# Optimization experiments

Hardware: AMD Instinct MI355X
Metric: run time of the kernel (lower is better)

## Reference

```python
import jax, jax.numpy as jnp
import numpy as np
from functools import partial

D_MODEL, D_INNER, D_STATE, DT_RANK, D_CONV, N_LAYER = 1024, 2048, 16, 64, 4, 4
OUT_DIM = 1024
EPS = 1e-5


def rmsnorm(x, w):
    return x * jax.lax.rsqrt(jnp.mean(x * x, axis=-1, keepdims=True) + EPS) * w


def causal_depthwise_conv(x, w, b):
    # x: [B, L, D]; w: [D, K]; depthwise causal conv along L
    xc = jnp.transpose(x, (0, 2, 1))  # [B, D, L]
    out = jax.lax.conv_general_dilated(
        xc, w[:, None, :],  # [D, 1, K]
        window_strides=(1,), padding=[(D_CONV - 1, 0)],
        dimension_numbers=('NCH', 'OIH', 'NCH'),
        feature_group_count=D_INNER)
    out = out + b[None, :, None]
    return jnp.transpose(out, (0, 2, 1))  # [B, L, D]


def selective_scan(u, delta, A, B, C, D):
    # u, delta: [b,l,d]; A: [d,n]; B,C: [b,l,n]; D: [d]
    def step(h, inp):
        d_t, B_t, C_t, u_t = inp  # [b,d],[b,n],[b,n],[b,d]
        dA = jnp.exp(d_t[..., None] * A)            # [b,d,n]
        h = dA * h + (d_t * u_t)[..., None] * B_t[:, None, :]
        y = jnp.einsum('bdn,bn->bd', h, C_t)
        return h, y
    b = u.shape[0]
    h0 = jnp.zeros((b, D_INNER, D_STATE), dtype=u.dtype)
    xs = (jnp.swapaxes(delta, 0, 1), jnp.swapaxes(B, 0, 1),
          jnp.swapaxes(C, 0, 1), jnp.swapaxes(u, 0, 1))
    _, ys = jax.lax.scan(step, h0, xs)
    y = jnp.swapaxes(ys, 0, 1)  # [b,l,d]
    return y + u * D


def mamba_block(x, in_w, conv_w, conv_b, xproj_w, dt_w, dt_b, A_log, D, out_w):
    xz = jnp.einsum('bld,ed->ble', x, in_w)            # [b,l,2*di]
    xp, z = jnp.split(xz, 2, axis=-1)
    xp = jax.nn.silu(causal_depthwise_conv(xp, conv_w, conv_b))
    x_dbl = jnp.einsum('bld,ed->ble', xp, xproj_w)      # [b,l,dt_rank+2n]
    dt, Bm, Cm = jnp.split(x_dbl, [DT_RANK, DT_RANK + D_STATE], axis=-1)
    delta = jax.nn.softplus(jnp.einsum('blr,dr->bld', dt, dt_w) + dt_b)
    A = -jnp.exp(A_log)
    y = selective_scan(xp, delta, A, Bm, Cm, D)
    y = y * jax.nn.silu(z)
    return jnp.einsum('bld,md->blm', y, out_w)


def setup_inputs() -> dict:
    key = jax.random.key(0)
    ks = jax.random.split(key, 16)
    s = 0.02
    x = jax.random.normal(ks[0], (2, 2048, D_MODEL), dtype=jnp.float32)
    emb_w = jax.random.normal(ks[1], (D_MODEL, D_MODEL), dtype=jnp.float32) * s
    emb_b = jnp.zeros((D_MODEL,), dtype=jnp.float32)
    L = N_LAYER
    in_proj_w = jax.random.normal(ks[2], (L, 2 * D_INNER, D_MODEL), dtype=jnp.float32) * s
    conv_w = jax.random.normal(ks[3], (L, D_INNER, D_CONV), dtype=jnp.float32) * 0.1
    conv_b = jnp.zeros((L, D_INNER), dtype=jnp.float32)
    x_proj_w = jax.random.normal(ks[4], (L, DT_RANK + 2 * D_STATE, D_INNER), dtype=jnp.float32) * s
    dt_proj_w = jax.random.normal(ks[5], (L, D_INNER, DT_RANK), dtype=jnp.float32) * s
    dt_proj_b = jax.random.uniform(ks[6], (L, D_INNER), dtype=jnp.float32, minval=-4.0, maxval=-2.0)
    A_log = jnp.broadcast_to(jnp.log(jnp.arange(1, D_STATE + 1, dtype=jnp.float32)), (L, D_INNER, D_STATE)).copy()
    D = jnp.ones((L, D_INNER), dtype=jnp.float32)
    out_proj_w = jax.random.normal(ks[7], (L, D_MODEL, D_INNER), dtype=jnp.float32) * s
    norm_w = jnp.ones((D_MODEL,), dtype=jnp.float32)
    head_w = jax.random.normal(ks[8], (OUT_DIM, D_MODEL), dtype=jnp.float32) * s
    return dict(x=x, emb_w=emb_w, emb_b=emb_b, in_proj_w=in_proj_w, conv_w=conv_w,
                conv_b=conv_b, x_proj_w=x_proj_w, dt_proj_w=dt_proj_w,
                dt_proj_b=dt_proj_b, A_log=A_log, D=D, out_proj_w=out_proj_w,
                norm_w=norm_w, head_w=head_w)


def reference(x, emb_w, emb_b, in_proj_w, conv_w, conv_b, x_proj_w, dt_proj_w,
              dt_proj_b, A_log, D, out_proj_w, norm_w, head_w):
    h = jnp.einsum('bli,di->bld', x, emb_w) + emb_b
    for i in range(N_LAYER):
        y = mamba_block(h, in_proj_w[i], conv_w[i], conv_b[i], x_proj_w[i],
                        dt_proj_w[i], dt_proj_b[i], A_log[i], D[i], out_proj_w[i])
        h = h + rmsnorm(y, norm_w)
    h = rmsnorm(h, norm_w)
    return jnp.einsum('bld,od->blo', h, head_w)
```

## Files before the change

### kernel.cpp

```cpp
#include <hip/hip_runtime.h>
#include <hip/hip_bf16.h>

#define DMODEL 1024
#define DINNER 2048
#define DSTATE 16
#define DTRANK 64
#define NLAYER 4
#define SEQ    2048
#define NB     2
#define BL     (NB*SEQ)

#define NCH   64
#define CLEN  (SEQ / NCH)

#define KSPLIT 8
#define NXD    96

typedef __bf16 bf16x8 __attribute__((ext_vector_type(8)));
typedef float  f32x4  __attribute__((ext_vector_type(4)));
typedef unsigned short u16x8 __attribute__((ext_vector_type(8)));

__device__ __forceinline__ unsigned short f2bf(float f) {
  unsigned int x = __builtin_bit_cast(unsigned int, f);
  x += 0x7fffu + ((x >> 16) & 1u);
  return (unsigned short)(x >> 16);
}
__device__ __forceinline__ float bf2f(unsigned short u) {
  unsigned int x = ((unsigned int)u) << 16;
  return __builtin_bit_cast(float, x);
}
__device__ __forceinline__ float siluf(float x) {
  return x * (1.f / (1.f + __expf(-x)));
}
__device__ __forceinline__ float softplusf(float x) {
  return (x > 15.f) ? x : __logf(1.f + __expf(x));
}

__device__ __forceinline__ void gload_lds16(const void* g, void* l) {
  __builtin_amdgcn_global_load_lds(
      (const __attribute__((address_space(1))) void*)g,
      (__attribute__((address_space(3))) void*)l, 16, 0, 0);
}

__device__ __forceinline__ void pack16(const float* p, u16x8& u0, u16x8& u1) {
  float4 f0 = *(const float4*)(p);
  float4 f1 = *(const float4*)(p + 4);
  float4 f2 = *(const float4*)(p + 8);
  float4 f3 = *(const float4*)(p + 12);
  u0[0]=f2bf(f0.x); u0[1]=f2bf(f0.y); u0[2]=f2bf(f0.z); u0[3]=f2bf(f0.w);
  u0[4]=f2bf(f1.x); u0[5]=f2bf(f1.y); u0[6]=f2bf(f1.z); u0[7]=f2bf(f1.w);
  u1[0]=f2bf(f2.x); u1[1]=f2bf(f2.y); u1[2]=f2bf(f2.z); u1[3]=f2bf(f2.w);
  u1[4]=f2bf(f3.x); u1[5]=f2bf(f3.y); u1[6]=f2bf(f3.z); u1[7]=f2bf(f3.w);
}

__global__ __launch_bounds__(512, 2) void gemm256(
    const unsigned short* __restrict__ A, int lda,
    const unsigned short* __restrict__ B, int ldb,
    unsigned short* __restrict__ Cbf, int ldc, int K)
{
  __shared__ alignas(16) unsigned short lds[3 * 16384];

  const int tid  = threadIdx.x;
  const int bm   = blockIdx.x, bn = blockIdx.y;
  const int wave = tid >> 6, lane = tid & 63;
  const int wm   = wave >> 2, wn = wave & 3;
  const int fr   = lane & 15, fq = lane >> 4;

  const int srow   = lane >> 2;
  const int schunk = (lane & 3) ^ ((lane >> 3) & 3);
  const unsigned short* Abase = A + (size_t)(bm * 256) * lda;
  const unsigned short* Bbase = B + (size_t)(bn * 256) * ldb;

  const int rc = fq ^ ((fr >> 1) & 3);

  f32x4 acc[8][4] = {};

#define STAGE256(t)                                                          \
  {                                                                          \
    char* sbase = (char*)lds + ((t) % 3) * 32768;                            \
    int k0 = (t) * 32;                                                       \
    _Pragma("unroll")                                                        \
    for (int r = 0; r < 2; ++r) {                                            \
      gload_lds16(Abase + (size_t)(r * 128 + wave * 16 + srow) * lda + k0 +  \
                      schunk * 8,                                            \
                  sbase + r * 8192 + wave * 1024);                           \
      gload_lds16(Bbase + (size_t)(r * 128 + wave * 16 + srow) * ldb + k0 +  \
                      schunk * 8,                                            \
                  sbase + 16384 + r * 8192 + wave * 1024);                   \
    }                                                                        \
  }

  const int NT = K >> 5;

  STAGE256(0);
  __builtin_amdgcn_sched_barrier(0);
  STAGE256(1);
  asm volatile("s_waitcnt vmcnt(4)" ::: "memory");
  __builtin_amdgcn_s_barrier();
  __builtin_amdgcn_sched_barrier(0);

  for (int t = 0; t < NT; ++t) {
    if (t + 2 < NT) STAGE256(t + 2);

    const char* bufp = (const char*)lds + (t % 3) * 32768;

    bf16x8 bfr[4];
#pragma unroll
    for (int nj = 0; nj < 4; ++nj)
      bfr[nj] = *(const bf16x8*)(bufp + 16384 +
                                 (wn * 64 + nj * 16 + fr) * 64 + rc * 16);
    __builtin_amdgcn_s_setprio(1);
#pragma unroll
    for (int mi = 0; mi < 8; ++mi) {
      bf16x8 af = *(const bf16x8*)(bufp + (wm * 128 + mi * 16 + fr) * 64 + rc * 16);
#pragma unroll
      for (int nj = 0; nj < 4; ++nj)
        acc[mi][nj] = __builtin_amdgcn_mfma_f32_16x16x32_bf16(af, bfr[nj], acc[mi][nj], 0, 0, 0);
    }
    __builtin_amdgcn_s_setprio(0);

    __builtin_amdgcn_sched_barrier(0);
    if (t + 2 < NT) {
      asm volatile("s_waitcnt vmcnt(4)" ::: "memory");
    } else if (t + 1 < NT) {
      asm volatile("s_waitcnt vmcnt(0)" ::: "memory");
    }
    __builtin_amdgcn_s_barrier();
    __builtin_amdgcn_sched_barrier(0);
  }
#undef STAGE256

#pragma unroll
  for (int mi = 0; mi < 8; ++mi)
#pragma unroll
    for (int nj = 0; nj < 4; ++nj)
#pragma unroll
      for (int q = 0; q < 4; ++q) {
        int row = bm * 256 + wm * 128 + mi * 16 + fq * 4 + q;
        int col = bn * 256 + wn * 64 + nj * 16 + fr;
        Cbf[(size_t)row * ldc + col] = f2bf(acc[mi][nj][q]);
      }
}

template<int ACT>
__global__ __launch_bounds__(256) void gemm_bf(
    const unsigned short* __restrict__ A, int lda,
    const unsigned short* __restrict__ B, int ldb,
    float* __restrict__ C, int ldc, int K,
    const float* __restrict__ bias,
    unsigned short* __restrict__ Cbf)
{
  __shared__ alignas(16) unsigned short ldsb[3 * 8192];

  const int tid  = threadIdx.x;
  const int bm   = blockIdx.x, bn = blockIdx.y;
  const int wave = tid >> 6,  lane = tid & 63;
  const int wm   = wave >> 1, wn   = wave & 1;
  const int fr   = lane & 15, fq   = lane >> 4;

  const int srow   = lane >> 2;
  const int schunk = (lane & 3) ^ ((lane >> 3) & 3);
  const unsigned short* Abase = A + (size_t)(bm * 128) * lda;
  const unsigned short* Bbase = B + (size_t)(bn * 128) * ldb;

  const int rc = fq ^ ((fr >> 1) & 3);

  f32x4 acc[4][4] = {};

#define STAGEP(t)                                                            \
  {                                                                          \
    char* sbase = (char*)ldsb + ((t) % 3) * 16384;                           \
    int k0 = (t) * 32;                                                       \
    _Pragma("unroll")                                                        \
    for (int j = 0; j < 2; ++j) {                                            \
      gload_lds16(Abase + (size_t)(wave * 32 + j * 16 + srow) * lda + k0 +   \
                      schunk * 8,                                            \
                  sbase + wave * 2048 + j * 1024);                           \
      gload_lds16(Bbase + (size_t)(wave * 32 + j * 16 + srow) * ldb + k0 +   \
                      schunk * 8,                                            \
                  sbase + 8192 + wave * 2048 + j * 1024);                    \
    }                                                                        \
  }

  const int NT = K >> 5;

  STAGEP(0);
  __builtin_amdgcn_sched_barrier(0);
  STAGEP(1);
  asm volatile("s_waitcnt vmcnt(4)" ::: "memory");
  __builtin_amdgcn_s_barrier();
  __builtin_amdgcn_sched_barrier(0);

  for (int t = 0; t < NT; ++t) {
    if (t + 2 < NT) STAGEP(t + 2);

    const char* bufp = (const char*)ldsb + (t % 3) * 16384;

    bf16x8 af[4], bfr[4];
#pragma unroll
    for (int mi = 0; mi < 4; ++mi)
      af[mi] = *(const bf16x8*)(bufp + (wm * 64 + mi * 16 + fr) * 64 + rc * 16);
#pragma unroll
    for (int nj = 0; nj < 4; ++nj)
      bfr[nj] = *(const bf16x8*)(bufp + 8192 +
                                 (wn * 64 + nj * 16 + fr) * 64 + rc * 16);
    __builtin_amdgcn_s_setprio(1);
#pragma unroll
    for (int mi = 0; mi < 4; ++mi)
#pragma unroll
      for (int nj = 0; nj < 4; ++nj)
        acc[mi][nj] = __builtin_amdgcn_mfma_f32_16x16x32_bf16(af[mi], bfr[nj], acc[mi][nj], 0, 0, 0);
    __builtin_amdgcn_s_setprio(0);

    __builtin_amdgcn_sched_barrier(0);
    if (t + 2 < NT) {
      asm volatile("s_waitcnt vmcnt(4)" ::: "memory");
    } else if (t + 1 < NT) {
      asm volatile("s_waitcnt vmcnt(0)" ::: "memory");
    }
    __builtin_amdgcn_s_barrier();
    __builtin_amdgcn_sched_barrier(0);
  }
#undef STAGEP

#pragma unroll
  for (int mi = 0; mi < 4; ++mi)
#pragma unroll
    for (int nj = 0; nj < 4; ++nj)
#pragma unroll
      for (int q = 0; q < 4; ++q) {
        int row = bm * 128 + wm * 64 + mi * 16 + fq * 4 + q;
        int col = bn * 128 + wn * 64 + nj * 16 + fr;
        float v = acc[mi][nj][q];
        if (bias) v += bias[col];
        if (ACT == 1) v = softplusf(v);
        if (C)   C[(size_t)row * ldc + col] = v;
        if (Cbf) Cbf[(size_t)row * ldc + col] = f2bf(v);
      }
}

__global__ __launch_bounds__(256) void gemm_xdbl(
    const unsigned short* __restrict__ A, const float* __restrict__ B,
    float* __restrict__ part)
{
  __shared__ alignas(16) unsigned short As[128 * 32];
  __shared__ alignas(16) unsigned short Bs[128 * 32];

  const int tid  = threadIdx.x;
  const int bm   = blockIdx.x;
  const int z    = blockIdx.z;
  const int wave = tid >> 6,  lane = tid & 63;
  const int wm   = wave >> 1, wn   = wave & 1;
  const int fr   = lane & 15, fq   = lane >> 4;

  const int r  = tid >> 1, hh = tid & 1;
  const int sw = (r & 7) << 4;
  const int offS0 = ((r * 64 + hh * 32)     ) ^ sw;
  const int offS1 = ((r * 64 + hh * 32 + 16)) ^ sw;

  const unsigned short* aRow = A + (size_t)(bm * 128 + r) * DINNER + hh * 16;
  const float* bRow = B + (size_t)r * DINNER + hh * 16;
  const bool bValid = (r < NXD);

  f32x4 acc[4][4] = {};

  const int kbeg = z * (DINNER / KSPLIT);
  for (int k0 = kbeg; k0 < kbeg + DINNER / KSPLIT; k0 += 32) {
    {
      u16x8 u0 = *(const u16x8*)(aRow + k0);
      u16x8 u1 = *(const u16x8*)(aRow + k0 + 8);
      *(u16x8*)((char*)As + offS0) = u0;
      *(u16x8*)((char*)As + offS1) = u1;
    }
    {
      u16x8 u0 = {}, u1 = {};
      if (bValid) pack16(bRow + k0, u0, u1);
      *(u16x8*)((char*)Bs + offS0) = u0;
      *(u16x8*)((char*)Bs + offS1) = u1;
    }
    __syncthreads();

    bf16x8 af[4], bfr[4];
#pragma unroll
    for (int mi = 0; mi < 4; ++mi) {
      int ra = wm * 64 + mi * 16 + fr;
      af[mi] = *(const bf16x8*)((const char*)As + ((ra * 64 + fq * 16) ^ ((ra & 7) << 4)));
    }
#pragma unroll
    for (int nj = 0; nj < 4; ++nj) {
      int rb = wn * 64 + nj * 16 + fr;
      bfr[nj] = *(const bf16x8*)((const char*)Bs + ((rb * 64 + fq * 16) ^ ((rb & 7) << 4)));
    }
#pragma unroll
    for (int mi = 0; mi < 4; ++mi)
#pragma unroll
      for (int nj = 0; nj < 4; ++nj)
        acc[mi][nj] = __builtin_amdgcn_mfma_f32_16x16x32_bf16(af[mi], bfr[nj], acc[mi][nj], 0, 0, 0);
    __syncthreads();
  }

#pragma unroll
  for (int mi = 0; mi < 4; ++mi)
#pragma unroll
    for (int nj = 0; nj < 4; ++nj)
#pragma unroll
      for (int q = 0; q < 4; ++q) {
        int row = bm * 128 + wm * 64 + mi * 16 + fq * 4 + q;
        int col = wn * 64 + nj * 16 + fr;
        if (col < NXD)
          part[((size_t)z * BL + row) * NXD + col] = acc[mi][nj][q];
      }
}

__global__ __launch_bounds__(256) void reduce_xdbl(
    const float* __restrict__ part, float* __restrict__ xdbl,
    unsigned short* __restrict__ xdbf)
{
  int i = blockIdx.x * 256 + threadIdx.x;
  float s = 0.f;
#pragma unroll
  for (int z = 0; z < KSPLIT; ++z) s += part[(size_t)z * BL * NXD + i];
  xdbl[i] = s;
  xdbf[i] = f2bf(s);
}

__global__ __launch_bounds__(256) void cvt_bf16(
    const float* __restrict__ in, unsigned short* __restrict__ out)
{
  int i = (blockIdx.x * 256 + threadIdx.x) * 4;
  float4 v = *(const float4*)(in + i);
  ushort4 o;
  o.x = f2bf(v.x); o.y = f2bf(v.y); o.z = f2bf(v.z); o.w = f2bf(v.w);
  *(ushort4*)(out + i) = o;
}

__global__ __launch_bounds__(256) void conv_silu_kernel(
    const unsigned short* __restrict__ xz, const float* __restrict__ cw,
    const float* __restrict__ cb, unsigned short* __restrict__ xpc)
{
  int idx = blockIdx.x * 256 + threadIdx.x;
  int dq  = idx & 511;
  int row = idx >> 9;
  int l   = row & (SEQ - 1);
  int d   = dq << 2;

  float4 bv = *(const float4*)(cb + d);
  float4 w0 = *(const float4*)(cw + (size_t)(d + 0) * 4);
  float4 w1 = *(const float4*)(cw + (size_t)(d + 1) * 4);
  float4 w2 = *(const float4*)(cw + (size_t)(d + 2) * 4);
  float4 w3 = *(const float4*)(cw + (size_t)(d + 3) * 4);

  float a0 = bv.x, a1 = bv.y, a2 = bv.z, a3 = bv.w;
#pragma unroll
  for (int k = 0; k < 4; ++k) {
    int ls = l - 3 + k;
    if (ls >= 0) {
      ushort4 xv = *(const ushort4*)(xz + (size_t)(row - 3 + k) * (2 * DINNER) + d);
      float x0 = bf2f(xv.x), x1 = bf2f(xv.y), x2 = bf2f(xv.z), x3 = bf2f(xv.w);
      float c0 = (k == 0) ? w0.x : (k == 1) ? w0.y : (k == 2) ? w0.z : w0.w;
      float c1 = (k == 0) ? w1.x : (k == 1) ? w1.y : (k == 2) ? w1.z : w1.w;
      float c2 = (k == 0) ? w2.x : (k == 1) ? w2.y : (k == 2) ? w2.z : w2.w;
      float c3 = (k == 0) ? w3.x : (k == 1) ? w3.y : (k == 2) ? w3.z : w3.w;
      a0 += x0 * c0; a1 += x1 * c1; a2 += x2 * c2; a3 += x3 * c3;
    }
  }
  ushort4 o;
  o.x = f2bf(siluf(a0)); o.y = f2bf(siluf(a1));
  o.z = f2bf(siluf(a2)); o.w = f2bf(siluf(a3));
  *(ushort4*)(xpc + (size_t)row * DINNER + d) = o;
}

__global__ __launch_bounds__(64) void scan_pass1(
    const unsigned short* __restrict__ dltb, const unsigned short* __restrict__ u_,
    const float* __restrict__ xd, const float* __restrict__ Alog,
    float* __restrict__ Sws, float* __restrict__ sdlws)
{
  int t = blockIdx.x * 64 + threadIdx.x;
  int d = t & (DINNER - 1);
  int cb = t >> 11;
  int c = cb & (NCH - 1);
  int b = cb >> 6;
  size_t r0 = (size_t)b * SEQ + (size_t)c * CLEN;

  float An0 = -__expf(Alog[(size_t)d * 16]);

  float S[16];
#pragma unroll
  for (int n = 0; n < 16; ++n) S[n] = 0.f;
  float sdl = 0.f;

  float dl = bf2f(dltb[r0 * DINNER + d]);
  float uu = bf2f(u_ [r0 * DINNER + d]);
  const float4* Bp0 = (const float4*)(xd + r0 * 96 + 64);
  float4 B0 = Bp0[0], B1 = Bp0[1], B2 = Bp0[2], B3 = Bp0[3];

#define P1_STEP                                                           \
  {                                                                       \
    float du = dl * uu;                                                   \
    sdl += dl;                                                            \
    float e1 = __expf(dl * An0);                                          \
    float Bv[16] = {B0.x,B0.y,B0.z,B0.w, B1.x,B1.y,B1.z,B1.w,             \
                    B2.x,B2.y,B2.z,B2.w, B3.x,B3.y,B3.z,B3.w};            \
    float p = e1;                                                         \
    _Pragma("unroll")                                                     \
    for (int n = 0; n < 16; ++n) {                                        \
      S[n] = p * S[n] + du * Bv[n];                                       \
      p *= e1;                                                            \
    }                                                                     \
  }

  for (int l = 0; l < CLEN - 1; ++l) {
    size_t rn = r0 + l + 1;
    float dln = bf2f(dltb[rn * DINNER + d]);
    float uun = bf2f(u_ [rn * DINNER + d]);
    const float4* Bp = (const float4*)(xd + rn * 96 + 64);
    float4 Bn0 = Bp[0], Bn1 = Bp[1], Bn2 = Bp[2], Bn3 = Bp[3];
    P1_STEP;
    dl = dln; uu = uun; B0 = Bn0; B1 = Bn1; B2 = Bn2; B3 = Bn3;
  }
  P1_STEP;
#undef P1_STEP

  size_t base = (size_t)cb * 16 * DINNER + d;
#pragma unroll
  for (int n = 0; n < 16; ++n) Sws[base + (size_t)n * DINNER] = S[n];
  sdlws[(size_t)cb * DINNER + d] = sdl;
}

__global__ __launch_bounds__(256) void scan_pass2(
    float* SH, const float* __restrict__ sdlws, const float* __restrict__ Alog)
{
  int t = blockIdx.x * 256 + threadIdx.x;
  int d = t & (DINNER - 1);
  int b = t >> 11;

  float An0 = -__expf(Alog[(size_t)d * 16]);

  float h[16];
#pragma unroll
  for (int n = 0; n < 16; ++n) h[n] = 0.f;

  for (int c = 0; c < NCH; ++c) {
    size_t bc = (size_t)(b * NCH + c);
    size_t base = bc * 16 * DINNER + d;
    float sdl = sdlws[bc * DINNER + d];
    float e1 = __expf(An0 * sdl);
    float Sc[16];
#pragma unroll
    for (int n = 0; n < 16; ++n) Sc[n] = SH[base + (size_t)n * DINNER];
#pragma unroll
    for (int n = 0; n < 16; ++n) SH[base + (size_t)n * DINNER] = h[n];
    float p = e1;
#pragma unroll
    for (int n = 0; n < 16; ++n) {
      h[n] = p * h[n] + Sc[n];
      p *= e1;
    }
  }
}

__global__ __launch_bounds__(64) void scan_pass3(
    const unsigned short* __restrict__ dltb,
    const unsigned short* __restrict__ u_,
    const float* __restrict__ xd,
    const unsigned short* __restrict__ xzb,
    const float* __restrict__ Alog,
    const float* __restrict__ Dv,
    const float* __restrict__ SH,
    unsigned short* __restrict__ ybf)
{
  int t = blockIdx.x * 64 + threadIdx.x;
  int d = t & (DINNER - 1);
  int cb = t >> 11;
  int c = cb & (NCH - 1);
  int b = cb >> 6;
  size_t r0 = (size_t)b * SEQ + (size_t)c * CLEN;

  float An0 = -__expf(Alog[(size_t)d * 16]);

  float h[16];
  {
    size_t base = (size_t)cb * 16 * DINNER + d;
#pragma unroll
    for (int n = 0; n < 16; ++n) h[n] = SH[base + (size_t)n * DINNER];
  }
  float Dd = Dv[d];

  float dl = bf2f(dltb[r0 * DINNER + d]);
  float uu = bf2f(u_ [r0 * DINNER + d]);
  float zz = bf2f(xzb[r0 * (2 * DINNER) + DINNER + d]);
  const float4* Xp0 = (const float4*)(xd + r0 * 96 + 64);
  float4 B0 = Xp0[0], B1 = Xp0[1], B2 = Xp0[2], B3 = Xp0[3];
  float4 C0 = Xp0[4], C1 = Xp0[5], C2 = Xp0[6], C3 = Xp0[7];

#define P3_STEP(RR)                                                       \
  {                                                                       \
    float Bv[16] = {B0.x,B0.y,B0.z,B0.w, B1.x,B1.y,B1.z,B1.w,             \
                    B2.x,B2.y,B2.z,B2.w, B3.x,B3.y,B3.z,B3.w};            \
    float Cv[16] = {C0.x,C0.y,C0.z,C0.w, C1.x,C1.y,C1.z,C1.w,             \
                    C2.x,C2.y,C2.z,C2.w, C3.x,C3.y,C3.z,C3.w};            \
    float du = dl * uu;                                                   \
    float e1 = __expf(dl * An0);                                          \
    float y0 = 0.f, y1 = 0.f;                                             \
    float p = e1;                                                         \
    _Pragma("unroll")                                                     \
    for (int n = 0; n < 16; n += 2) {                                     \
      h[n]   = p * h[n]   + du * Bv[n];   y0 += h[n]   * Cv[n];           \
      p *= e1;                                                            \
      h[n+1] = p * h[n+1] + du * Bv[n+1]; y1 += h[n+1] * Cv[n+1];         \
      p *= e1;                                                            \
    }                                                                     \
    float y = y0 + y1;                                                    \
    ybf[(RR) * DINNER + d] = f2bf((y + uu * Dd) * siluf(zz));             \
  }

  for (int l = 0; l < CLEN - 1; ++l) {
    size_t rn = r0 + l + 1;
    float dln = bf2f(dltb[rn * DINNER + d]);
    float uun = bf2f(u_ [rn * DINNER + d]);
    float zzn = bf2f(xzb[rn * (2 * DINNER) + DINNER + d]);
    const float4* Xp = (const float4*)(xd + rn * 96 + 64);
    float4 Bn0 = Xp[0], Bn1 = Xp[1], Bn2 = Xp[2], Bn3 = Xp[3];
    float4 Cn0 = Xp[4], Cn1 = Xp[5], Cn2 = Xp[6], Cn3 = Xp[7];
    P3_STEP(r0 + l);
    dl = dln; uu = uun; zz = zzn;
    B0 = Bn0; B1 = Bn1; B2 = Bn2; B3 = Bn3;
    C0 = Cn0; C1 = Cn1; C2 = Cn2; C3 = Cn3;
  }
  P3_STEP(r0 + CLEN - 1);
#undef P3_STEP
}

template<int ADDRES, int WF32, int WBF>
__global__ __launch_bounds__(256) void rmsnorm_kernel(
    const float* __restrict__ x, const float* __restrict__ w,
    const float* __restrict__ res, float* __restrict__ out,
    unsigned short* __restrict__ outbf)
{
  int row = blockIdx.x, tid = threadIdx.x;
  float4 v = *(const float4*)(x + (size_t)row * DMODEL + tid * 4);
  float ss = v.x * v.x + v.y * v.y + v.z * v.z + v.w * v.w;
#pragma unroll
  for (int off = 32; off > 0; off >>= 1) ss += __shfl_xor(ss, off);
  __shared__ float sb[4];
  if ((tid & 63) == 0) sb[tid >> 6] = ss;
  __syncthreads();
  ss = (sb[0] + sb[1]) + (sb[2] + sb[3]);
  float sc = rsqrtf(ss * (1.f / DMODEL) + 1e-5f);
  float4 wv = *(const float4*)(w + tid * 4);
  float4 o;
  o.x = v.x * sc * wv.x; o.y = v.y * sc * wv.y;
  o.z = v.z * sc * wv.z; o.w = v.w * sc * wv.w;
  if (ADDRES) {
    float4 rv = *(const float4*)(res + (size_t)row * DMODEL + tid * 4);
    o.x += rv.x; o.y += rv.y; o.z += rv.z; o.w += rv.w;
  }
  if (WF32) *(float4*)(out + (size_t)row * DMODEL + tid * 4) = o;
  if (WBF) {
    ushort4 ob;
    ob.x = f2bf(o.x); ob.y = f2bf(o.y); ob.z = f2bf(o.z); ob.w = f2bf(o.w);
    *(ushort4*)(outbf + (size_t)row * DMODEL + tid * 4) = ob;
  }
}

extern "C" void kernel_launch(void* const* d_in, const int* in_sizes, int n_in,
                              void* d_out, int out_size, void* d_ws, size_t ws_size,
                              hipStream_t stream) {
  const float* x        = (const float*)d_in[0];
  const float* emb_w    = (const float*)d_in[1];
  const float* emb_b    = (const float*)d_in[2];
  const float* in_projw = (const float*)d_in[3];
  const float* conv_w   = (const float*)d_in[4];
  const float* conv_b   = (const float*)d_in[5];
  const float* x_projw  = (const float*)d_in[6];
  const float* dt_projw = (const float*)d_in[7];
  const float* dt_projb = (const float*)d_in[8];
  const float* A_log    = (const float*)d_in[9];
  const float* Dvec     = (const float*)d_in[10];
  const float* out_projw= (const float*)d_in[11];
  const float* norm_w   = (const float*)d_in[12];
  const float* head_w   = (const float*)d_in[13];

  float* ws = (float*)d_ws;
  float* h    = ws;
  unsigned short* xzb = (unsigned short*)(h + (size_t)BL * DMODEL);
  unsigned short* xpcb= xzb + (size_t)BL * 2 * DINNER;
  unsigned short* dltb= xpcb+ (size_t)BL * DINNER;
  float* xdbl = (float*)(dltb + (size_t)BL * DINNER);
  float* SH   = xdbl + (size_t)BL * NXD;
  float* sdlw = SH   + (size_t)NB * NCH * 16 * DINNER;
  float* part = sdlw + (size_t)NB * NCH * DINNER;
  unsigned short* hbf = (unsigned short*)(part + (size_t)KSPLIT * BL * NXD);
  unsigned short* ybf = hbf + (size_t)BL * DMODEL;
  unsigned short* wA  = ybf + (size_t)BL * DINNER;
  unsigned short* wB  = wA  + (size_t)2 * DINNER * DMODEL;
  unsigned short* xdbf= (unsigned short*)(SH + (size_t)NB * NCH * 16 * DINNER
                                             - (size_t)(BL * NXD + DINNER * DTRANK) / 2);
  unsigned short* wdt = xdbf + (size_t)BL * NXD;
  unsigned short* xbf = (unsigned short*)part;
  float* tmp  = (float*)xzb;

  dim3 blk(256);

  cvt_bf16<<<dim3(BL * DMODEL / 1024), blk, 0, stream>>>(x, xbf);
  cvt_bf16<<<dim3(DMODEL * DMODEL / 1024), blk, 0, stream>>>(emb_w, wA);
  gemm_bf<0><<<dim3(BL / 128, DMODEL / 128), blk, 0, stream>>>(
      xbf, DMODEL, wA, DMODEL, h, DMODEL, DMODEL, emb_b, hbf);

  for (int i = 0; i < NLAYER; ++i) {
    const float* in_w = in_projw + (size_t)i * 2 * DINNER * DMODEL;
    const float* cw   = conv_w   + (size_t)i * DINNER * 4;
    const float* cb   = conv_b   + (size_t)i * DINNER;
    const float* xpw  = x_projw  + (size_t)i * NXD * DINNER;
    const float* dtw  = dt_projw + (size_t)i * DINNER * DTRANK;
    const float* dtb  = dt_projb + (size_t)i * DINNER;
    const float* Al   = A_log    + (size_t)i * DINNER * DSTATE;
    const float* Dl   = Dvec     + (size_t)i * DINNER;
    const float* ow   = out_projw+ (size_t)i * DMODEL * DINNER;

    cvt_bf16<<<dim3(2 * DINNER * DMODEL / 1024), blk, 0, stream>>>(in_w, wA);
    gemm256<<<dim3(BL / 256, (2 * DINNER) / 256), dim3(512), 0, stream>>>(
        hbf, DMODEL, wA, DMODEL, xzb, 2 * DINNER, DMODEL);
    conv_silu_kernel<<<dim3(BL * (DINNER / 4) / 256), blk, 0, stream>>>(xzb, cw, cb, xpcb);
    gemm_xdbl<<<dim3(BL / 128, 1, KSPLIT), blk, 0, stream>>>(xpcb, xpw, part);
    reduce_xdbl<<<dim3(BL * NXD / 256), blk, 0, stream>>>(part, xdbl, xdbf);
    cvt_bf16<<<dim3(DINNER * DTRANK / 1024), blk, 0, stream>>>(dtw, wdt);
    gemm_bf<1><<<dim3(BL / 128, DINNER / 128), blk, 0, stream>>>(
        xdbf, NXD, wdt, DTRANK, nullptr, DINNER, DTRANK, dtb, dltb);
    scan_pass1<<<dim3(NB * NCH * DINNER / 64), dim3(64), 0, stream>>>(
        dltb, xpcb, xdbl, Al, SH, sdlw);
    scan_pass2<<<dim3(NB * DINNER / 256), blk, 0, stream>>>(SH, sdlw, Al);
    scan_pass3<<<dim3(NB * NCH * DINNER / 64), dim3(64), 0, stream>>>(
        dltb, xpcb, xdbl, xzb, Al, Dl, SH, ybf);
    cvt_bf16<<<dim3(DMODEL * DINNER / 1024), blk, 0, stream>>>(ow, wB);
    gemm_bf<0><<<dim3(BL / 128, DMODEL / 128), blk, 0, stream>>>(
        ybf, DINNER, wB, DINNER, tmp, DMODEL, DINNER, nullptr, nullptr);
    rmsnorm_kernel<1, 1, 1><<<dim3(BL), blk, 0, stream>>>(tmp, norm_w, h, h, hbf);
  }

  rmsnorm_kernel<0, 0, 1><<<dim3(BL), blk, 0, stream>>>(h, norm_w, nullptr, nullptr, hbf);
  cvt_bf16<<<dim3(DMODEL * DMODEL / 1024), blk, 0, stream>>>(head_w, wA);
  gemm_bf<0><<<dim3(BL / 128, DMODEL / 128), blk, 0, stream>>>(
      hbf, DMODEL, wA, DMODEL, (float*)d_out, DMODEL, DMODEL, nullptr, nullptr);
}
```

Before: 1.086 ms.

## Store scan chunk states in bf16 and batch all weight conversions upfront

Chunk-level scan states passed between the three scan passes are now stored as bf16 instead of fp32, halving the workspace traffic for the inter-chunk state exchange. All per-layer weight conversions to bf16 are also hoisted into a few large launches at the start, with separate buffers per layer, so fewer small kernels run inside the layer loop. The workspace layout is rearranged to fit the larger weight buffers. Rounding the carried scan state to bf16 costs precision in the recurrence.

```diff
diff --git a/kernel.cpp b/kernel.cpp
--- a/kernel.cpp
+++ b/kernel.cpp
@@ -373,7 +373,7 @@
 __global__ __launch_bounds__(64) void scan_pass1(
     const unsigned short* __restrict__ dltb, const unsigned short* __restrict__ u_,
     const float* __restrict__ xd, const float* __restrict__ Alog,
-    float* __restrict__ Sws, float* __restrict__ sdlws)
+    unsigned short* __restrict__ Sws, float* __restrict__ sdlws)
 {
   int t = blockIdx.x * 64 + threadIdx.x;
   int d = t & (DINNER - 1);
@@ -423,12 +423,13 @@
 
   size_t base = (size_t)cb * 16 * DINNER + d;
 #pragma unroll
-  for (int n = 0; n < 16; ++n) Sws[base + (size_t)n * DINNER] = S[n];
+  for (int n = 0; n < 16; ++n) Sws[base + (size_t)n * DINNER] = f2bf(S[n]);
   sdlws[(size_t)cb * DINNER + d] = sdl;
 }
 
 __global__ __launch_bounds__(256) void scan_pass2(
-    float* SH, const float* __restrict__ sdlws, const float* __restrict__ Alog)
+    unsigned short* SH, const float* __restrict__ sdlws,
+    const float* __restrict__ Alog)
 {
   int t = blockIdx.x * 256 + threadIdx.x;
   int d = t & (DINNER - 1);
@@ -447,9 +448,9 @@
     float e1 = __expf(An0 * sdl);
     float Sc[16];
 #pragma unroll
-    for (int n = 0; n < 16; ++n) Sc[n] = SH[base + (size_t)n * DINNER];
-#pragma unroll
-    for (int n = 0; n < 16; ++n) SH[base + (size_t)n * DINNER] = h[n];
+    for (int n = 0; n < 16; ++n) Sc[n] = bf2f(SH[base + (size_t)n * DINNER]);
+#pragma unroll
+    for (int n = 0; n < 16; ++n) SH[base + (size_t)n * DINNER] = f2bf(h[n]);
     float p = e1;
 #pragma unroll
     for (int n = 0; n < 16; ++n) {
@@ -466,7 +467,7 @@
     const unsigned short* __restrict__ xzb,
     const float* __restrict__ Alog,
     const float* __restrict__ Dv,
-    const float* __restrict__ SH,
+    const unsigned short* __restrict__ SH,
     unsigned short* __restrict__ ybf)
 {
   int t = blockIdx.x * 64 + threadIdx.x;
@@ -482,7 +483,7 @@
   {
     size_t base = (size_t)cb * 16 * DINNER + d;
 #pragma unroll
-    for (int n = 0; n < 16; ++n) h[n] = SH[base + (size_t)n * DINNER];
+    for (int n = 0; n < 16; ++n) h[n] = bf2f(SH[base + (size_t)n * DINNER]);
   }
   float Dd = Dv[d];
 
@@ -587,59 +588,61 @@
   unsigned short* xpcb= xzb + (size_t)BL * 2 * DINNER;
   unsigned short* dltb= xpcb+ (size_t)BL * DINNER;
   float* xdbl = (float*)(dltb + (size_t)BL * DINNER);
-  float* SH   = xdbl + (size_t)BL * NXD;
-  float* sdlw = SH   + (size_t)NB * NCH * 16 * DINNER;
+  unsigned short* SHb = (unsigned short*)(xdbl + (size_t)BL * NXD);
+  float* sdlw = (float*)(SHb + (size_t)NB * NCH * 16 * DINNER);
   float* part = sdlw + (size_t)NB * NCH * DINNER;
   unsigned short* hbf = (unsigned short*)(part + (size_t)KSPLIT * BL * NXD);
   unsigned short* ybf = hbf + (size_t)BL * DMODEL;
-  unsigned short* wA  = ybf + (size_t)BL * DINNER;
-  unsigned short* wB  = wA  + (size_t)2 * DINNER * DMODEL;
-  unsigned short* xdbf= (unsigned short*)(SH + (size_t)NB * NCH * 16 * DINNER
-                                             - (size_t)(BL * NXD + DINNER * DTRANK) / 2);
-  unsigned short* wdt = xdbf + (size_t)BL * NXD;
+  unsigned short* wInAll  = ybf + (size_t)BL * DINNER;
+  unsigned short* wOutAll = wInAll + (size_t)NLAYER * 2 * DINNER * DMODEL;
+  unsigned short* wDtAll  = wOutAll + (size_t)NLAYER * DMODEL * DINNER;
+  unsigned short* wEmb    = wDtAll + (size_t)NLAYER * DINNER * DTRANK;
+  unsigned short* wHead   = wEmb + (size_t)DMODEL * DMODEL;
+  unsigned short* xdbf= SHb + (size_t)NB * NCH * 16 * DINNER - (size_t)BL * NXD;
   unsigned short* xbf = (unsigned short*)part;
   float* tmp  = (float*)xzb;
 
   dim3 blk(256);
 
   cvt_bf16<<<dim3(BL * DMODEL / 1024), blk, 0, stream>>>(x, xbf);
-  cvt_bf16<<<dim3(DMODEL * DMODEL / 1024), blk, 0, stream>>>(emb_w, wA);
+  cvt_bf16<<<dim3(DMODEL * DMODEL / 1024), blk, 0, stream>>>(emb_w, wEmb);
+  cvt_bf16<<<dim3(NLAYER * 2 * DINNER * DMODEL / 1024), blk, 0, stream>>>(in_projw, wInAll);
+  cvt_bf16<<<dim3(NLAYER * DMODEL * DINNER / 1024), blk, 0, stream>>>(out_projw, wOutAll);
+  cvt_bf16<<<dim3(NLAYER * DINNER * DTRANK / 1024), blk, 0, stream>>>(dt_projw, wDtAll);
+  cvt_bf16<<<dim3(DMODEL * DMODEL / 1024), blk, 0, stream>>>(head_w, wHead);
+
   gemm_bf<0><<<dim3(BL / 128, DMODEL / 128), blk, 0, stream>>>(
-      xbf, DMODEL, wA, DMODEL, h, DMODEL, DMODEL, emb_b, hbf);
+      xbf, DMODEL, wEmb, DMODEL, h, DMODEL, DMODEL, emb_b, hbf);
 
   for (int i = 0; i < NLAYER; ++i) {
-    const float* in_w = in_projw + (size_t)i * 2 * DINNER * DMODEL;
+    const unsigned short* wA = wInAll  + (size_t)i * 2 * DINNER * DMODEL;
+    const unsigned short* wB = wOutAll + (size_t)i * DMODEL * DINNER;
+    const unsigned short* wd = wDtAll  + (size_t)i * DINNER * DTRANK;
     const float* cw   = conv_w   + (size_t)i * DINNER * 4;
     const float* cb   = conv_b   + (size_t)i * DINNER;
     const float* xpw  = x_projw  + (size_t)i * NXD * DINNER;
-    const float* dtw  = dt_projw + (size_t)i * DINNER * DTRANK;
     const float* dtb  = dt_projb + (size_t)i * DINNER;
     const float* Al   = A_log    + (size_t)i * DINNER * DSTATE;
     const float* Dl   = Dvec     + (size_t)i * DINNER;
-    const float* ow   = out_projw+ (size_t)i * DMODEL * DINNER;
-
-    cvt_bf16<<<dim3(2 * DINNER * DMODEL / 1024), blk, 0, stream>>>(in_w, wA);
+
     gemm256<<<dim3(BL / 256, (2 * DINNER) / 256), dim3(512), 0, stream>>>(
         hbf, DMODEL, wA, DMODEL, xzb, 2 * DINNER, DMODEL);
     conv_silu_kernel<<<dim3(BL * (DINNER / 4) / 256), blk, 0, stream>>>(xzb, cw, cb, xpcb);
     gemm_xdbl<<<dim3(BL / 128, 1, KSPLIT), blk, 0, stream>>>(xpcb, xpw, part);
     reduce_xdbl<<<dim3(BL * NXD / 256), blk, 0, stream>>>(part, xdbl, xdbf);
-    cvt_bf16<<<dim3(DINNER * DTRANK / 1024), blk, 0, stream>>>(dtw, wdt);
     gemm_bf<1><<<dim3(BL / 128, DINNER / 128), blk, 0, stream>>>(
-        xdbf, NXD, wdt, DTRANK, nullptr, DINNER, DTRANK, dtb, dltb);
+        xdbf, NXD, wd, DTRANK, nullptr, DINNER, DTRANK, dtb, dltb);
     scan_pass1<<<dim3(NB * NCH * DINNER / 64), dim3(64), 0, stream>>>(
-        dltb, xpcb, xdbl, Al, SH, sdlw);
-    scan_pass2<<<dim3(NB * DINNER / 256), blk, 0, stream>>>(SH, sdlw, Al);
+        dltb, xpcb, xdbl, Al, SHb, sdlw);
+    scan_pass2<<<dim3(NB * DINNER / 256), blk, 0, stream>>>(SHb, sdlw, Al);
     scan_pass3<<<dim3(NB * NCH * DINNER / 64), dim3(64), 0, stream>>>(
-        dltb, xpcb, xdbl, xzb, Al, Dl, SH, ybf);
-    cvt_bf16<<<dim3(DMODEL * DINNER / 1024), blk, 0, stream>>>(ow, wB);
+        dltb, xpcb, xdbl, xzb, Al, Dl, SHb, ybf);
     gemm_bf<0><<<dim3(BL / 128, DMODEL / 128), blk, 0, stream>>>(
         ybf, DINNER, wB, DINNER, tmp, DMODEL, DINNER, nullptr, nullptr);
     rmsnorm_kernel<1, 1, 1><<<dim3(BL), blk, 0, stream>>>(tmp, norm_w, h, h, hbf);
   }
 
   rmsnorm_kernel<0, 0, 1><<<dim3(BL), blk, 0, stream>>>(h, norm_w, nullptr, nullptr, hbf);
-  cvt_bf16<<<dim3(DMODEL * DMODEL / 1024), blk, 0, stream>>>(head_w, wA);
   gemm_bf<0><<<dim3(BL / 128, DMODEL / 128), blk, 0, stream>>>(
-      hbf, DMODEL, wA, DMODEL, (float*)d_out, DMODEL, DMODEL, nullptr, nullptr);
-}
+      hbf, DMODEL, wHead, DMODEL, (float*)d_out, DMODEL, DMODEL, nullptr, nullptr);
+}
```

Measured after the change: 1.064 ms. 2.0% less time.
